# Optimization experiments

Hardware: AMD Instinct MI355X
Metric: run time of the kernel (lower is better)

## Reference

```python
import jax, jax.numpy as jnp
import numpy as np

B, N, D, C = 1, 512, 128, 128
EPS = 1e-5


def _layernorm(x, g, b):
    m = jnp.mean(x, axis=-1, keepdims=True)
    v = jnp.mean(jnp.square(x - m), axis=-1, keepdims=True)
    return (x - m) * jax.lax.rsqrt(v + EPS) * g + b


def setup_inputs() -> dict:
    key = jax.random.key(0)
    ks = jax.random.split(key, 14)
    sD = 1.0 / np.sqrt(D)
    sC = 1.0 / np.sqrt(C)

    def w(k, shape, scale):
        return jax.random.normal(k, shape, dtype=jnp.float32) * scale

    return {
        "x": jax.random.normal(ks[0], (B, N, N, D), dtype=jnp.float32),
        "ln_in_g": jnp.ones((D,), jnp.float32),
        "ln_in_b": jnp.zeros((D,), jnp.float32),
        "ln_out_g": jnp.ones((C,), jnp.float32),
        "ln_out_b": jnp.zeros((C,), jnp.float32),
        "Wl": w(ks[1], (D, C), sD), "bl": w(ks[2], (C,), 0.02),
        "Wr": w(ks[3], (D, C), sD), "br": w(ks[4], (C,), 0.02),
        "Wo": w(ks[5], (C, D), sC), "bo": w(ks[6], (D,), 0.02),
        "Wlg": w(ks[7], (D, C), sD), "blg": w(ks[8], (C,), 0.02),
        "Wrg": w(ks[9], (D, C), sD), "brg": w(ks[10], (C,), 0.02),
        "Wog": w(ks[11], (D, D), sD), "bog": w(ks[12], (D,), 0.02),
    }


def reference(x, ln_in_g, ln_in_b, ln_out_g, ln_out_b,
              Wl, bl, Wr, br, Wo, bo, Wlg, blg, Wrg, brg, Wog, bog):
    # x: [B, N, N, D] pair representation
    xn = _layernorm(x, ln_in_g, ln_in_b)
    left = jax.nn.sigmoid(xn @ Wlg + blg) * (xn @ Wl + bl)    # [B,N,N,C]
    right = jax.nn.sigmoid(xn @ Wrg + brg) * (xn @ Wr + br)   # [B,N,N,C]
    # type='out': contract over k (rows): out[b,i,j,c] = sum_k left[b,k,i,c]*right[b,k,j,c]
    out = jnp.einsum('bkic,bkjc->bijc', left, right)           # [B,N,N,C]
    out = jax.nn.sigmoid(xn @ Wog + bog) * (_layernorm(out, ln_out_g, ln_out_b) @ Wo + bo)
    return out
```

## Files before the change

kernel.cpp:

```cpp
#include <hip/hip_runtime.h>
#include <hip/hip_bf16.h>
#include <cstdint>
#include <cstddef>

typedef unsigned short u16;
typedef short bf16x8 __attribute__((ext_vector_type(8)));
typedef float f32x4 __attribute__((ext_vector_type(4)));

constexpr int Ns = 512;
constexpr int Dd = 128;
constexpr int Cc = 128;
#define EPSV 1e-5f

__device__ __forceinline__ u16 f2bf(float f){
    __hip_bfloat16 h = __float2bfloat16(f);
    return *reinterpret_cast<u16*>(&h);
}
__device__ __forceinline__ float bf2f(u16 h){
    return __uint_as_float(((uint32_t)h) << 16);
}
__device__ __forceinline__ float sigmoidf_(float x){
    return 1.0f / (1.0f + __expf(-x));
}

__global__ void k_prep(const float* __restrict__ Wl, const float* __restrict__ Wlg,
                       const float* __restrict__ Wr, const float* __restrict__ Wrg,
                       const float* __restrict__ Wog, const float* __restrict__ Wo,
                       u16* __restrict__ Wt){
    int idx = blockIdx.x * 256 + threadIdx.x;
    if (idx >= 6 * 16384) return;
    int m = idx >> 14; int nk = idx & 16383; int n = nk >> 7; int k = nk & 127;
    const float* W = (m == 0) ? Wl : (m == 1) ? Wlg : (m == 2) ? Wr
                   : (m == 3) ? Wrg : (m == 4) ? Wog : Wo;
    Wt[idx] = f2bf(W[k * Cc + n]);
}

__global__ __launch_bounds__(256) void k1(
    const float* __restrict__ x, const float* __restrict__ g_ln, const float* __restrict__ b_ln,
    const u16* __restrict__ Wt,
    const float* __restrict__ bl, const float* __restrict__ blg,
    const float* __restrict__ br, const float* __restrict__ brg,
    const float* __restrict__ bog,
    u16* __restrict__ left, u16* __restrict__ right, u16* __restrict__ og)
{
    __shared__ u16  lA[64][136];
    __shared__ u16  lSbuf[9216];
    __shared__ float gln[128], bln[128];

    const int t   = threadIdx.x;
    const int bid = blockIdx.x;
    const int a0  = (bid >> 6) << 3;
    const int b0  = (bid & 63) << 3;
    if (t < 128){ gln[t] = g_ln[t]; bln[t] = b_ln[t]; }

    const int r = t >> 2, q = t & 3;
    const int aa = a0 + (r & 7), bb = b0 + (r >> 3);
    const float4* xrow = reinterpret_cast<const float4*>(x + ((size_t)aa * Ns + bb) * Dd);
    float4 xv[8];
    float s1 = 0.f, s2 = 0.f;
#pragma unroll
    for (int i2 = 0; i2 < 8; ++i2){
        float4 v = xrow[q + 4 * i2];
        xv[i2] = v;
        s1 += v.x + v.y + v.z + v.w;
        s2 += v.x * v.x + v.y * v.y + v.z * v.z + v.w * v.w;
    }
    s1 += __shfl_xor(s1, 1); s1 += __shfl_xor(s1, 2);
    s2 += __shfl_xor(s2, 1); s2 += __shfl_xor(s2, 2);
    const float mm  = s1 * (1.0f / 128.0f);
    const float rsv = rsqrtf(s2 * (1.0f / 128.0f) - mm * mm + EPSV);
    __syncthreads();
    {
#pragma unroll
        for (int i2 = 0; i2 < 8; ++i2){
            const int d = (q + 4 * i2) * 4;
            ushort4 o;
            o.x = f2bf((xv[i2].x - mm) * rsv * gln[d + 0] + bln[d + 0]);
            o.y = f2bf((xv[i2].y - mm) * rsv * gln[d + 1] + bln[d + 1]);
            o.z = f2bf((xv[i2].z - mm) * rsv * gln[d + 2] + bln[d + 2]);
            o.w = f2bf((xv[i2].w - mm) * rsv * gln[d + 3] + bln[d + 3]);
            *reinterpret_cast<ushort4*>(&lA[r][d]) = o;
        }
    }
    __syncthreads();

    const int w = t >> 6, l = t & 63;
    const int lrow = l & 15, lk = (l >> 4) << 3;
    const int nb = w * 32;
    const int orow = (l >> 4) << 2;
    const size_t kb = (size_t)(a0 >> 3);
    const f32x4 zero4 = {0.f, 0.f, 0.f, 0.f};

#pragma unroll 1
    for (int pair = 0; pair < 2; ++pair){
        const u16* WV = Wt + (size_t)(pair * 2 + 0) * 16384;
        const u16* WG = Wt + (size_t)(pair * 2 + 1) * 16384;
        const float* bV = pair ? br : bl;
        const float* bG = pair ? brg : blg;
        u16* dst = pair ? right : left;
        f32x4 accV[4][2], accG[4][2];
#pragma unroll
        for (int rf = 0; rf < 4; ++rf)
#pragma unroll
            for (int cf = 0; cf < 2; ++cf){ accV[rf][cf] = zero4; accG[rf][cf] = zero4; }
#pragma unroll
        for (int ks = 0; ks < 4; ++ks){
            const int k0 = ks * 32 + lk;
            bf16x8 af[4];
#pragma unroll
            for (int rf = 0; rf < 4; ++rf)
                af[rf] = *reinterpret_cast<const bf16x8*>(&lA[rf * 16 + lrow][k0]);
#pragma unroll
            for (int cf = 0; cf < 2; ++cf){
                const int col = nb + cf * 16 + lrow;
                bf16x8 bv = *reinterpret_cast<const bf16x8*>(WV + (size_t)col * 128 + k0);
                bf16x8 bg = *reinterpret_cast<const bf16x8*>(WG + (size_t)col * 128 + k0);
#pragma unroll
                for (int rf = 0; rf < 4; ++rf){
                    accV[rf][cf] = __builtin_amdgcn_mfma_f32_16x16x32_bf16(af[rf], bv, accV[rf][cf], 0, 0, 0);
                    accG[rf][cf] = __builtin_amdgcn_mfma_f32_16x16x32_bf16(af[rf], bg, accG[rf][cf], 0, 0, 0);
                }
            }
        }
#pragma unroll
        for (int cf = 0; cf < 2; ++cf){
            const int col = nb + cf * 16 + lrow;
            const float bVv = bV[col], bGv = bG[col];
#pragma unroll
            for (int rf = 0; rf < 4; ++rf){
                ushort4 pk;
#pragma unroll
                for (int j = 0; j < 4; ++j){
                    const float vv = accV[rf][cf][j] + bVv;
                    const float gg = accG[rf][cf][j] + bGv;
                    ((u16*)&pk)[j] = f2bf(sigmoidf_(gg) * vv);
                }
                *reinterpret_cast<ushort4*>(&lSbuf[(size_t)(w * 32 + cf * 16 + lrow) * 72 + rf * 16 + orow]) = pk;
            }
        }
#pragma unroll
        for (int it = 0; it < 4; ++it){
            const int cl = it * 8 + (l >> 3);
            const int chunk = l & 7;
            const int cg = nb + cl;
            int4 vdat = *reinterpret_cast<const int4*>(&lSbuf[(size_t)(w * 32 + cl) * 72 + chunk * 8]);
            size_t base = (((size_t)cg * 64 + kb) * Ns + b0) * 8 + (size_t)chunk * 8;
            *reinterpret_cast<int4*>(dst + base) = vdat;
        }
    }

    __syncthreads();

    {
        const u16* WO = Wt + (size_t)4 * 16384;
        f32x4 acc[4][2];
#pragma unroll
        for (int rf = 0; rf < 4; ++rf)
#pragma unroll
            for (int cf = 0; cf < 2; ++cf) acc[rf][cf] = zero4;
#pragma unroll
        for (int ks = 0; ks < 4; ++ks){
            const int k0 = ks * 32 + lk;
            bf16x8 af[4];
#pragma unroll
            for (int rf = 0; rf < 4; ++rf)
                af[rf] = *reinterpret_cast<const bf16x8*>(&lA[rf * 16 + lrow][k0]);
#pragma unroll
            for (int cf = 0; cf < 2; ++cf){
                bf16x8 bv = *reinterpret_cast<const bf16x8*>(WO + (size_t)(nb + cf * 16 + lrow) * 128 + k0);
#pragma unroll
                for (int rf = 0; rf < 4; ++rf)
                    acc[rf][cf] = __builtin_amdgcn_mfma_f32_16x16x32_bf16(af[rf], bv, acc[rf][cf], 0, 0, 0);
            }
        }
#pragma unroll
        for (int cf = 0; cf < 2; ++cf){
            const int col = nb + cf * 16 + lrow;
            const float bOv = bog[col];
#pragma unroll
            for (int rf = 0; rf < 4; ++rf){
#pragma unroll
                for (int j = 0; j < 4; ++j){
                    const int row = rf * 16 + orow + j;
                    lSbuf[(size_t)row * 132 + col] = f2bf(sigmoidf_(acc[rf][cf][j] + bOv));
                }
            }
        }
        __syncthreads();
        const int bsub = t >> 5, c4 = (t & 31) * 4;
#pragma unroll
        for (int a = 0; a < 8; ++a){
            const int row = bsub * 8 + a;
            int2 v = *reinterpret_cast<const int2*>(&lSbuf[(size_t)row * 132 + c4]);
            *reinterpret_cast<int2*>(og + (((size_t)(a0 + a) * Ns) + (b0 + bsub)) * Cc + c4) = v;
        }
    }
}

#define K2_LOAD(AF, BF, KS) do {                                                    \
    const size_t kbrow_ = (size_t)((KS) * 4 + lkb) * Ns;                            \
    _Pragma("unroll") for (int rf = 0; rf < 4; ++rf)                                \
        AF[rf] = *reinterpret_cast<const bf16x8*>(Lc + (kbrow_ + ib + rf * 16 + lrow) * 8); \
    _Pragma("unroll") for (int cf = 0; cf < 4; ++cf)                                \
        BF[cf] = *reinterpret_cast<const bf16x8*>(Rc + (kbrow_ + jb + cf * 16 + lrow) * 8); \
} while (0)

#define K2_MM(AF, BF) do {                                                          \
    _Pragma("unroll") for (int rf = 0; rf < 4; ++rf)                                \
    _Pragma("unroll") for (int cf = 0; cf < 4; ++cf)                                \
        acc[rf][cf] = __builtin_amdgcn_mfma_f32_16x16x32_bf16(AF[rf], BF[cf], acc[rf][cf], 0, 0, 0); \
} while (0)

__global__ __launch_bounds__(256) void k2(const u16* __restrict__ left,
                                          const u16* __restrict__ right,
                                          u16* __restrict__ om)
{
    __shared__ u16 sO[128][136];
    const int bid = blockIdx.x;
    const int xcd = bid & 7, idxx = bid >> 3;
    const int virt = xcd * 256 + idxx;
    const int c    = virt >> 4;
    const int tile = virt & 15;
    const int iy = tile >> 2, jx = tile & 3;
    const int t = threadIdx.x, w = t >> 6, l = t & 63;
    const int wr = w >> 1, wc = w & 1;
    const int ib = iy * 128 + wr * 64;
    const int jb = jx * 128 + wc * 64;
    const int lrow = l & 15, lkb = l >> 4;
    const u16* Lc = left  + (size_t)c * (Ns * Ns);
    const u16* Rc = right + (size_t)c * (Ns * Ns);
    const f32x4 zero4 = {0.f, 0.f, 0.f, 0.f};
    f32x4 acc[4][4];
#pragma unroll
    for (int rf = 0; rf < 4; ++rf)
#pragma unroll
        for (int cf = 0; cf < 4; ++cf) acc[rf][cf] = zero4;

    bf16x8 a0f[4], b0f[4], a1f[4], b1f[4];
    K2_LOAD(a0f, b0f, 0);
#pragma unroll
    for (int ks = 0; ks < 16; ks += 2){
        K2_LOAD(a1f, b1f, ks + 1);
        K2_MM(a0f, b0f);
        if (ks + 2 < 16) K2_LOAD(a0f, b0f, ks + 2);
        K2_MM(a1f, b1f);
    }

    const int orow = (l >> 4) << 2;
#pragma unroll
    for (int rf = 0; rf < 4; ++rf)
#pragma unroll
        for (int j2 = 0; j2 < 4; ++j2){
            const int rloc = wr * 64 + rf * 16 + orow + j2;
#pragma unroll
            for (int cf = 0; cf < 4; ++cf)
                sO[rloc][wc * 64 + cf * 16 + lrow] = f2bf(acc[rf][cf][j2]);
        }
    __syncthreads();
    u16* obase = om + (size_t)c * Ns * Ns + (size_t)(iy * 128) * Ns + jx * 128;
#pragma unroll
    for (int s = 0; s < 8; ++s){
        const int g = s * 256 + t;
        const int row = g >> 4, co = (g & 15) * 8;
        int4 v = *reinterpret_cast<const int4*>(&sO[row][co]);
        *reinterpret_cast<int4*>(obase + (size_t)row * Ns + co) = v;
    }
}

__global__ __launch_bounds__(256) void k3(
    const u16* __restrict__ om, const u16* __restrict__ og, const u16* __restrict__ Wt,
    const float* __restrict__ g2, const float* __restrict__ b2, const float* __restrict__ bo,
    float* __restrict__ out)
{
    __shared__ char smem[34816];
    u16* X = reinterpret_cast<u16*>(smem);
    u16* O = reinterpret_cast<u16*>(smem) + 8704;
    __shared__ float sg2[128], sb2[128];
    const int i  = blockIdx.y;
    const int j0 = blockIdx.x * 64;
    const int t  = threadIdx.x;
    if (t < 128){ sg2[t] = g2[t]; sb2[t] = b2[t]; }
    {
        const int c = t >> 1, jh = (t & 1) * 32;
        const u16* src = om + (size_t)c * Ns * Ns + (size_t)i * Ns + j0 + jh;
#pragma unroll
        for (int s = 0; s < 8; ++s){
            ushort4 v = reinterpret_cast<const ushort4*>(src)[s];
            const int jj = jh + s * 4;
            X[(jj + 0) * 136 + c] = v.x; X[(jj + 1) * 136 + c] = v.y;
            X[(jj + 2) * 136 + c] = v.z; X[(jj + 3) * 136 + c] = v.w;
        }
    }
    {
        const int jj = t >> 2, qq = t & 3;
        const u16* src = og + ((size_t)i * Ns + j0 + jj) * Cc + qq * 32;
#pragma unroll
        for (int s = 0; s < 4; ++s)
            *reinterpret_cast<int4*>(&O[jj * 136 + qq * 32 + s * 8]) = reinterpret_cast<const int4*>(src)[s];
    }
    __syncthreads();
    const int r = t >> 2, q = t & 3;
    {
        float s1 = 0.f, s2v = 0.f;
#pragma unroll
        for (int e = 0; e < 32; ++e){
            const float v = bf2f(X[r * 136 + q * 32 + e]);
            s1 += v; s2v += v * v;
        }
        s1  += __shfl_xor(s1, 1);  s1  += __shfl_xor(s1, 2);
        s2v += __shfl_xor(s2v, 1); s2v += __shfl_xor(s2v, 2);
        const float mm  = s1 * (1.0f / 128.0f);
        const float rsv = rsqrtf(s2v * (1.0f / 128.0f) - mm * mm + EPSV);
#pragma unroll
        for (int e = 0; e < 32; ++e){
            const int cc = q * 32 + e;
            const float v = bf2f(X[r * 136 + cc]);
            X[r * 136 + cc] = f2bf((v - mm) * rsv * sg2[cc] + sb2[cc]);
        }
    }
    __syncthreads();
    const int w = t >> 6, l = t & 63;
    const int lrow = l & 15, lk = (l >> 4) << 3, nbv = w * 32, orow = (l >> 4) << 2;
    const u16* WO = Wt + (size_t)5 * 16384;
    const f32x4 zero4 = {0.f, 0.f, 0.f, 0.f};
    f32x4 acc[4][2];
#pragma unroll
    for (int rf = 0; rf < 4; ++rf)
#pragma unroll
        for (int cf = 0; cf < 2; ++cf) acc[rf][cf] = zero4;
#pragma unroll
    for (int ks = 0; ks < 4; ++ks){
        const int k0 = ks * 32 + lk;
        bf16x8 af[4];
#pragma unroll
        for (int rf = 0; rf < 4; ++rf)
            af[rf] = *reinterpret_cast<const bf16x8*>(&X[(rf * 16 + lrow) * 136 + k0]);
#pragma unroll
        for (int cf = 0; cf < 2; ++cf){
            bf16x8 bv = *reinterpret_cast<const bf16x8*>(WO + (size_t)(nbv + cf * 16 + lrow) * 128 + k0);
#pragma unroll
            for (int rf = 0; rf < 4; ++rf)
                acc[rf][cf] = __builtin_amdgcn_mfma_f32_16x16x32_bf16(af[rf], bv, acc[rf][cf], 0, 0, 0);
        }
    }
    float gv[2][4][4];
#pragma unroll
    for (int cf = 0; cf < 2; ++cf){
        const int cg = nbv + cf * 16 + lrow;
        const float bov = bo[cg];
#pragma unroll
        for (int rf = 0; rf < 4; ++rf)
#pragma unroll
            for (int j = 0; j < 4; ++j){
                const int row = rf * 16 + orow + j;
                gv[cf][rf][j] = bf2f(O[row * 136 + cg]) * (acc[rf][cf][j] + bov);
            }
    }
    __syncthreads();
    float* sF = reinterpret_cast<float*>(smem);
#pragma unroll
    for (int cf = 0; cf < 2; ++cf){
        const int cg = nbv + cf * 16 + lrow;
#pragma unroll
        for (int rf = 0; rf < 4; ++rf)
#pragma unroll
            for (int j = 0; j < 4; ++j){
                const int row = rf * 16 + orow + j;
                sF[row * 128 + cg] = gv[cf][rf][j];
            }
    }
    __syncthreads();
    const float4* sF4 = reinterpret_cast<const float4*>(smem);
    float* obase = out + ((size_t)i * Ns + j0) * Cc;
#pragma unroll
    for (int s = 0; s < 8; ++s){
        const int g = s * 256 + t;
        const int row = g >> 5, co = (g & 31) * 4;
        float4 v = sF4[g];
        *reinterpret_cast<float4*>(obase + (size_t)row * Cc + co) = v;
    }
}

extern "C" void kernel_launch(void* const* d_in, const int* in_sizes, int n_in,
                              void* d_out, int out_size, void* d_ws, size_t ws_size,
                              hipStream_t stream)
{
    const float* x    = (const float*)d_in[0];
    const float* ling = (const float*)d_in[1];
    const float* linb = (const float*)d_in[2];
    const float* loutg= (const float*)d_in[3];
    const float* loutb= (const float*)d_in[4];
    const float* Wl   = (const float*)d_in[5];
    const float* bl   = (const float*)d_in[6];
    const float* Wr   = (const float*)d_in[7];
    const float* br   = (const float*)d_in[8];
    const float* Wo   = (const float*)d_in[9];
    const float* bo   = (const float*)d_in[10];
    const float* Wlg  = (const float*)d_in[11];
    const float* blg  = (const float*)d_in[12];
    const float* Wrg  = (const float*)d_in[13];
    const float* brg  = (const float*)d_in[14];
    const float* Wog  = (const float*)d_in[15];
    const float* bog  = (const float*)d_in[16];

    char* ws = (char*)d_ws;
    u16* Wt = (u16*)ws;
    const size_t off = 256 * 1024;
    const size_t SZ  = (size_t)33554432 * 2;
    u16* left  = (u16*)(ws + off);
    u16* right = (u16*)(ws + off + SZ);
    u16* og    = (u16*)(ws + off + 2 * SZ);
    u16* om    = (u16*)(ws + off + 3 * SZ);

    hipLaunchKernelGGL(k_prep, dim3(384), dim3(256), 0, stream, Wl, Wlg, Wr, Wrg, Wog, Wo, Wt);
    hipLaunchKernelGGL(k1, dim3(4096), dim3(256), 0, stream,
                       x, ling, linb, Wt, bl, blg, br, brg, bog, left, right, og);
    hipLaunchKernelGGL(k2, dim3(2048), dim3(256), 0, stream, left, right, om);
    hipLaunchKernelGGL(k3, dim3(8, 512), dim3(256), 0, stream, om, og, Wt, loutg, loutb, bo, (float*)d_out);
}
```

Baseline: 277.5 us.

## Cut k1 register pressure and write left/right projections directly to global

```diff
diff --git a/kernel.cpp b/kernel.cpp
--- a/kernel.cpp
+++ b/kernel.cpp
@@ -35,7 +35,7 @@
     Wt[idx] = f2bf(W[k * Cc + n]);
 }
 
-__global__ __launch_bounds__(256) void k1(
+__global__ __launch_bounds__(256, 3) void k1(
     const float* __restrict__ x, const float* __restrict__ g_ln, const float* __restrict__ b_ln,
     const u16* __restrict__ Wt,
     const float* __restrict__ bl, const float* __restrict__ blg,
@@ -44,7 +44,7 @@
     u16* __restrict__ left, u16* __restrict__ right, u16* __restrict__ og)
 {
     __shared__ u16  lA[64][136];
-    __shared__ u16  lSbuf[9216];
+    __shared__ u16  lS[64][132];
     __shared__ float gln[128], bln[128];
 
     const int t   = threadIdx.x;
@@ -88,8 +88,15 @@
     const int lrow = l & 15, lk = (l >> 4) << 3;
     const int nb = w * 32;
     const int orow = (l >> 4) << 2;
-    const size_t kb = (size_t)(a0 >> 3);
+    const int kb = a0 >> 3;
     const f32x4 zero4 = {0.f, 0.f, 0.f, 0.f};
+
+    bf16x8 af[4][4];
+#pragma unroll
+    for (int ks = 0; ks < 4; ++ks)
+#pragma unroll
+        for (int rf = 0; rf < 4; ++rf)
+            af[ks][rf] = *reinterpret_cast<const bf16x8*>(&lA[rf * 16 + lrow][ks * 32 + lk]);
 
 #pragma unroll 1
     for (int pair = 0; pair < 2; ++pair){
@@ -98,91 +105,64 @@
         const float* bV = pair ? br : bl;
         const float* bG = pair ? brg : blg;
         u16* dst = pair ? right : left;
-        f32x4 accV[4][2], accG[4][2];
-#pragma unroll
-        for (int rf = 0; rf < 4; ++rf)
-#pragma unroll
-            for (int cf = 0; cf < 2; ++cf){ accV[rf][cf] = zero4; accG[rf][cf] = zero4; }
-#pragma unroll
-        for (int ks = 0; ks < 4; ++ks){
-            const int k0 = ks * 32 + lk;
-            bf16x8 af[4];
-#pragma unroll
-            for (int rf = 0; rf < 4; ++rf)
-                af[rf] = *reinterpret_cast<const bf16x8*>(&lA[rf * 16 + lrow][k0]);
-#pragma unroll
-            for (int cf = 0; cf < 2; ++cf){
-                const int col = nb + cf * 16 + lrow;
+
+#pragma unroll 1
+        for (int cf = 0; cf < 2; ++cf){
+            const int col = nb + cf * 16 + lrow;
+            f32x4 accV[4], accG[4];
+#pragma unroll
+            for (int rf = 0; rf < 4; ++rf){ accV[rf] = zero4; accG[rf] = zero4; }
+#pragma unroll
+            for (int ks = 0; ks < 4; ++ks){
+                const int k0 = ks * 32 + lk;
                 bf16x8 bv = *reinterpret_cast<const bf16x8*>(WV + (size_t)col * 128 + k0);
                 bf16x8 bg = *reinterpret_cast<const bf16x8*>(WG + (size_t)col * 128 + k0);
 #pragma unroll
-                for (int rf = 0; rf < 4; ++rf){
-                    accV[rf][cf] = __builtin_amdgcn_mfma_f32_16x16x32_bf16(af[rf], bv, accV[rf][cf], 0, 0, 0);
-                    accG[rf][cf] = __builtin_amdgcn_mfma_f32_16x16x32_bf16(af[rf], bg, accG[rf][cf], 0, 0, 0);
+                for (int rf = 0; rf < 4; ++rf)
+                    accV[rf] = __builtin_amdgcn_mfma_f32_16x16x32_bf16(af[ks][rf], bv, accV[rf], 0, 0, 0);
+#pragma unroll
+                for (int rf = 0; rf < 4; ++rf)
+                    accG[rf] = __builtin_amdgcn_mfma_f32_16x16x32_bf16(af[ks][rf], bg, accG[rf], 0, 0, 0);
+            }
+            const float bVv = bV[col], bGv = bG[col];
+#pragma unroll
+            for (int rf = 0; rf < 4; ++rf){
+                ushort4 pk;
+#pragma unroll
+                for (int j = 0; j < 4; ++j){
+                    const float vv = accV[rf][j] + bVv;
+                    const float gg = accG[rf][j] + bGv;
+                    ((u16*)&pk)[j] = f2bf(sigmoidf_(gg) * vv);
                 }
-            }
-        }
-#pragma unroll
+                const size_t base = (((size_t)col * 64 + kb) * Ns + b0 + rf * 2 + (orow >> 3)) * 8 + (orow & 4);
+                *reinterpret_cast<ushort4*>(dst + base) = pk;
+            }
+        }
+    }
+
+    {
+        const u16* WO = Wt + (size_t)4 * 16384;
+#pragma unroll 1
         for (int cf = 0; cf < 2; ++cf){
             const int col = nb + cf * 16 + lrow;
-            const float bVv = bV[col], bGv = bG[col];
-#pragma unroll
-            for (int rf = 0; rf < 4; ++rf){
-                ushort4 pk;
-#pragma unroll
-                for (int j = 0; j < 4; ++j){
-                    const float vv = accV[rf][cf][j] + bVv;
-                    const float gg = accG[rf][cf][j] + bGv;
-                    ((u16*)&pk)[j] = f2bf(sigmoidf_(gg) * vv);
-                }
-                *reinterpret_cast<ushort4*>(&lSbuf[(size_t)(w * 32 + cf * 16 + lrow) * 72 + rf * 16 + orow]) = pk;
-            }
-        }
-#pragma unroll
-        for (int it = 0; it < 4; ++it){
-            const int cl = it * 8 + (l >> 3);
-            const int chunk = l & 7;
-            const int cg = nb + cl;
-            int4 vdat = *reinterpret_cast<const int4*>(&lSbuf[(size_t)(w * 32 + cl) * 72 + chunk * 8]);
-            size_t base = (((size_t)cg * 64 + kb) * Ns + b0) * 8 + (size_t)chunk * 8;
-            *reinterpret_cast<int4*>(dst + base) = vdat;
-        }
-    }
-
-    __syncthreads();
-
-    {
-        const u16* WO = Wt + (size_t)4 * 16384;
-        f32x4 acc[4][2];
-#pragma unroll
-        for (int rf = 0; rf < 4; ++rf)
-#pragma unroll
-            for (int cf = 0; cf < 2; ++cf) acc[rf][cf] = zero4;
-#pragma unroll
-        for (int ks = 0; ks < 4; ++ks){
-            const int k0 = ks * 32 + lk;
-            bf16x8 af[4];
-#pragma unroll
-            for (int rf = 0; rf < 4; ++rf)
-                af[rf] = *reinterpret_cast<const bf16x8*>(&lA[rf * 16 + lrow][k0]);
-#pragma unroll
-            for (int cf = 0; cf < 2; ++cf){
-                bf16x8 bv = *reinterpret_cast<const bf16x8*>(WO + (size_t)(nb + cf * 16 + lrow) * 128 + k0);
+            f32x4 acc[4];
+#pragma unroll
+            for (int rf = 0; rf < 4; ++rf) acc[rf] = zero4;
+#pragma unroll
+            for (int ks = 0; ks < 4; ++ks){
+                const int k0 = ks * 32 + lk;
+                bf16x8 bv = *reinterpret_cast<const bf16x8*>(WO + (size_t)col * 128 + k0);
 #pragma unroll
                 for (int rf = 0; rf < 4; ++rf)
-                    acc[rf][cf] = __builtin_amdgcn_mfma_f32_16x16x32_bf16(af[rf], bv, acc[rf][cf], 0, 0, 0);
-            }
-        }
-#pragma unroll
-        for (int cf = 0; cf < 2; ++cf){
-            const int col = nb + cf * 16 + lrow;
+                    acc[rf] = __builtin_amdgcn_mfma_f32_16x16x32_bf16(af[ks][rf], bv, acc[rf], 0, 0, 0);
+            }
             const float bOv = bog[col];
 #pragma unroll
             for (int rf = 0; rf < 4; ++rf){
 #pragma unroll
                 for (int j = 0; j < 4; ++j){
                     const int row = rf * 16 + orow + j;
-                    lSbuf[(size_t)row * 132 + col] = f2bf(sigmoidf_(acc[rf][cf][j] + bOv));
+                    lS[row][col] = f2bf(sigmoidf_(acc[rf][j] + bOv));
                 }
             }
         }
@@ -191,7 +171,7 @@
 #pragma unroll
         for (int a = 0; a < 8; ++a){
             const int row = bsub * 8 + a;
-            int2 v = *reinterpret_cast<const int2*>(&lSbuf[(size_t)row * 132 + c4]);
+            int2 v = *reinterpret_cast<const int2*>(&lS[row][c4]);
             *reinterpret_cast<int2*>(og + (((size_t)(a0 + a) * Ns) + (b0 + bsub)) * Cc + c4) = v;
         }
     }
```

Measured after the change: 272.8 us. No clear change (-1.7%).
